# Kernel tuning notes

Hardware: AMD Instinct MI355X
Metric: run time of the kernel (lower is better)

The kernel has to match this reference:

```python
import jax, jax.numpy as jnp
import numpy as np

N = 100000; E = 1600000; F_NODE = 64; F_EDGE = 16
H = 4; C = 32; HC = H * C  # heads=4, per-head out=32, concat dim 128
NG = 64; NCLS = 10
DIMS_IN = [F_NODE, HC, HC]


def _init_params(key):
    ps = {}
    ks = iter(jax.random.split(key, 40))
    for i, din in enumerate(DIMS_IN, 1):
        ps[f"W{i}"] = jax.random.normal(next(ks), (din, HC), jnp.float32) / np.sqrt(din).astype(np.float32)
        ps[f"aS{i}"] = jax.random.normal(next(ks), (H, C), jnp.float32) / np.sqrt(C).astype(np.float32)
        ps[f"aD{i}"] = jax.random.normal(next(ks), (H, C), jnp.float32) / np.sqrt(C).astype(np.float32)
        ps[f"We{i}"] = jax.random.normal(next(ks), (F_EDGE, HC), jnp.float32) / np.sqrt(F_EDGE).astype(np.float32)
        ps[f"aE{i}"] = jax.random.normal(next(ks), (H, C), jnp.float32) / np.sqrt(C).astype(np.float32)
        ps[f"b{i}"] = jnp.zeros((HC,), jnp.float32)
    ps["Wc1"] = jax.random.normal(next(ks), (HC, 128), jnp.float32) / np.sqrt(HC).astype(np.float32)
    ps["bc1"] = jnp.zeros((128,), jnp.float32)
    ps["Wc2"] = jax.random.normal(next(ks), (128, NCLS), jnp.float32) / np.sqrt(128).astype(np.float32)
    ps["bc2"] = jnp.zeros((NCLS,), jnp.float32)
    ps["Wl1"] = jax.random.normal(next(ks), (HC, 64), jnp.float32) / np.sqrt(HC).astype(np.float32)
    ps["bl1"] = jnp.zeros((64,), jnp.float32)
    ps["Wl2"] = jax.random.normal(next(ks), (64, 1), jnp.float32) / np.sqrt(64).astype(np.float32)
    ps["bl2"] = jnp.zeros((1,), jnp.float32)
    return ps


def setup_inputs() -> dict:
    key = jax.random.key(0)
    kx, ke, ki, kb, kp = jax.random.split(key, 5)
    inp = {
        "x": jax.random.normal(kx, (N, F_NODE), jnp.float32),
        "edge_index": jax.random.randint(ki, (2, E), 0, N, dtype=jnp.int64) if jax.config.jax_enable_x64 else jax.random.randint(ki, (2, E), 0, N),
        "edge_attr": jax.random.normal(ke, (E, F_EDGE), jnp.float32),
        "batch": jnp.sort(jax.random.randint(kb, (N,), 0, NG)),
    }
    inp.update(_init_params(kp))
    return inp


def _gat(x, src, dst, ea, W, aS, aD, We, aE, b):
    # One PyG-style GATConv (concat=True, eval mode, self-loops already added).
    n = x.shape[0]
    h = (x @ W).reshape(n, H, C)                    # [N,H,C]
    e = (ea @ We).reshape(-1, H, C)                 # [E',H,C]
    ls = jnp.einsum("nhc,hc->nh", h, aS)            # alpha_src per node
    ld = jnp.einsum("nhc,hc->nh", h, aD)            # alpha_dst per node
    le = jnp.einsum("ehc,hc->eh", e, aE)            # alpha_edge per edge
    logits = jax.nn.leaky_relu(ls[src] + ld[dst] + le, 0.2)  # [E',H]
    m = jax.ops.segment_max(logits, dst, num_segments=n)
    m = jnp.where(jnp.isfinite(m), m, 0.0)          # guard empty segments
    ex = jnp.exp(logits - m[dst])
    den = jax.ops.segment_sum(ex, dst, num_segments=n) + 1e-16
    alpha = ex / den[dst]                           # segment softmax over dst
    out = jax.ops.segment_sum(h[src] * alpha[..., None], dst, num_segments=n)
    return out.reshape(n, HC) + b


def reference(x, edge_index, edge_attr, batch, W1, aS1, aD1, We1, aE1, b1, W2, aS2, aD2, We2, aE2, b2, W3, aS3, aD3, We3, aE3, b3, Wc1, bc1, Wc2, bc2, Wl1, bl1, Wl2, bl2):
    n = x.shape[0]
    loop = jnp.arange(n, dtype=edge_index.dtype)
    src = jnp.concatenate([edge_index[0], loop])
    dst = jnp.concatenate([edge_index[1], loop])
    # self-loop edge_attr filled with mean of edge_attr (PyG fill_value='mean')
    ea = jnp.concatenate([edge_attr, jnp.broadcast_to(edge_attr.mean(0), (n, edge_attr.shape[1]))], 0)
    h = jax.nn.elu(_gat(x, src, dst, ea, W1, aS1, aD1, We1, aE1, b1))
    h = jax.nn.elu(_gat(h, src, dst, ea, W2, aS2, aD2, We2, aE2, b2))
    h = _gat(h, src, dst, ea, W3, aS3, aD3, We3, aE3, b3)
    loc_logits = (jax.nn.relu(h @ Wl1 + bl1) @ Wl2 + bl2)[:, 0]
    cnt = jax.ops.segment_sum(jnp.ones((n,), x.dtype), batch, num_segments=NG)
    gemb = jax.ops.segment_sum(h, batch, num_segments=NG) / jnp.maximum(cnt, 1.0)[:, None]
    class_logits = jax.nn.relu(gemb @ Wc1 + bc1) @ Wc2 + bc2
    return class_logits, loc_logits
```

## Files before the change

kernel.cpp:

```cpp
#include <hip/hip_runtime.h>
#include <math.h>


constexpr int SCAN_TILE = 2048;
constexpr int DEG_CAP = 128;

__global__ void init_cnt_kernel(int* cnt, float* mean_acc, int n) {
  int i = blockIdx.x * blockDim.x + threadIdx.x;
  if (i < n) cnt[i] = 1;
  if (blockIdx.x == 0 && threadIdx.x < 16) mean_acc[threadIdx.x] = 0.f;
}

__global__ void count_kernel(const int* __restrict__ dst, int* cnt, int E) {
  int stride = gridDim.x * blockDim.x;
  for (int e = blockIdx.x * blockDim.x + threadIdx.x; e < E; e += stride)
    atomicAdd(&cnt[dst[e]], 1);
}

__global__ void scan1_kernel(const int* __restrict__ cnt, int* rowptr, int* bsum, int n) {
  __shared__ int part[256];
  int t = threadIdx.x, b = blockIdx.x;
  int base = b * SCAN_TILE + t * 8;
  int v[8];
  int s = 0;
#pragma unroll
  for (int i = 0; i < 8; ++i) {
    int idx = base + i;
    v[i] = (idx < n) ? cnt[idx] : 0;
    s += v[i];
  }
  part[t] = s;
  __syncthreads();
  if (t == 0) {
    int run = 0;
    for (int i = 0; i < 256; ++i) { int x = part[i]; part[i] = run; run += x; }
    bsum[b] = run;
  }
  __syncthreads();
  int run = part[t];
#pragma unroll
  for (int i = 0; i < 8; ++i) {
    int idx = base + i;
    run += v[i];
    if (idx < n) rowptr[idx + 1] = run;
  }
}

__global__ void scan2_kernel(int* bsum, int nb, int* rowptr) {
  if (threadIdx.x == 0 && blockIdx.x == 0) {
    rowptr[0] = 0;
    int run = 0;
    for (int b = 0; b < nb; ++b) { int x = bsum[b]; bsum[b] = run; run += x; }
  }
}

__global__ void scan3_kernel(const int* __restrict__ bsum, int* rowptr, int* cursor, int n) {
  int off = bsum[blockIdx.x];
  int base = blockIdx.x * SCAN_TILE + threadIdx.x * 8;
#pragma unroll
  for (int i = 0; i < 8; ++i) {
    int idx = base + i;
    if (idx < n) {
      int v = rowptr[idx + 1] + off;
      rowptr[idx + 1] = v;
      if (idx + 1 < n) cursor[idx + 1] = v;
    }
  }
  if (blockIdx.x == 0 && threadIdx.x == 0) cursor[0] = 0;
}

__global__ void scatter_kernel(const int* __restrict__ ei, int* cursor,
                               int* esrc, int* eeid, int E, int n) {
  int stride = gridDim.x * blockDim.x;
  int total = E + n;
  for (int i = blockIdx.x * blockDim.x + threadIdx.x; i < total; i += stride) {
    int s, d, id;
    if (i < E) { s = ei[i]; d = ei[E + i]; id = i; }
    else       { s = i - E; d = s; id = E; }
    int pos = atomicAdd(&cursor[d], 1);
    esrc[pos] = s;
    eeid[pos] = id;
  }
}

template <bool MEAN>
__global__ void le_kernel(const float* __restrict__ ea, const float* __restrict__ We,
                          const float* __restrict__ aE, float* __restrict__ le,
                          float* __restrict__ m_acc, int E) {
  __shared__ float wr[16][4];
  int t = threadIdx.x;
  if (t < 64) {
    int f = t >> 2, h = t & 3;
    float s = 0.f;
    for (int c = 0; c < 32; ++c) s += We[f * 128 + h * 32 + c] * aE[h * 32 + c];
    wr[f][h] = s;
  }
  __syncthreads();
  float a[16];
  if (MEAN) {
#pragma unroll
    for (int i = 0; i < 16; ++i) a[i] = 0.f;
  }
  int stride = gridDim.x * blockDim.x;
  for (int e = blockIdx.x * blockDim.x + t; e < E; e += stride) {
    const float4* p = (const float4*)(ea + (size_t)e * 16);
    float4 x0 = p[0], x1 = p[1], x2 = p[2], x3 = p[3];
    float xf[16] = {x0.x, x0.y, x0.z, x0.w, x1.x, x1.y, x1.z, x1.w,
                    x2.x, x2.y, x2.z, x2.w, x3.x, x3.y, x3.z, x3.w};
    if (MEAN) {
#pragma unroll
      for (int i = 0; i < 16; ++i) a[i] += xf[i];
    }
    float oo[4];
#pragma unroll
    for (int h = 0; h < 4; ++h) {
      float s = 0.f;
#pragma unroll
      for (int f = 0; f < 16; ++f) s += xf[f] * wr[f][h];
      oo[h] = s;
    }
    *(float4*)(le + (size_t)e * 4) = make_float4(oo[0], oo[1], oo[2], oo[3]);
  }
  if (MEAN) {
    __shared__ float sm[16];
    if (t < 16) sm[t] = 0.f;
    __syncthreads();
#pragma unroll
    for (int i = 0; i < 16; ++i) atomicAdd(&sm[i], a[i]);
    __syncthreads();
    if (t < 16) atomicAdd(&m_acc[t], sm[t]);
  }
}

__global__ void le_self_kernel(const float* __restrict__ mean_acc, float scale,
                               const float* __restrict__ We, const float* __restrict__ aE,
                               float* __restrict__ le, int E) {
  __shared__ float wr[16][4];
  int t = threadIdx.x;
  if (t < 64) {
    int f = t >> 2, h = t & 3;
    float s = 0.f;
    for (int c = 0; c < 32; ++c) s += We[f * 128 + h * 32 + c] * aE[h * 32 + c];
    wr[f][h] = s;
  }
  __syncthreads();
  if (t < 4) {
    float s = 0.f;
    for (int f = 0; f < 16; ++f) s += mean_acc[f] * scale * wr[f][t];
    le[(size_t)E * 4 + t] = s;
  }
}

template <int K>
__global__ __launch_bounds__(128) void proj_kernel(
    const float* __restrict__ in, const float* __restrict__ W,
    const float* __restrict__ aS, const float* __restrict__ aD,
    float* __restrict__ hp, float* __restrict__ ls, float* __restrict__ ldv, int n) {
  __shared__ float xs[8][K];
  int t = threadIdx.x;
  int base = blockIdx.x * 8;
  for (int idx = t; idx < 8 * K; idx += 128) {
    int r = idx / K, k = idx - r * K;
    int row = base + r;
    xs[r][k] = (row < n) ? in[(size_t)row * K + k] : 0.f;
  }
  __syncthreads();
  float acc[8];
#pragma unroll
  for (int r = 0; r < 8; ++r) acc[r] = 0.f;
  for (int k = 0; k < K; ++k) {
    float w = W[k * 128 + t];
#pragma unroll
    for (int r = 0; r < 8; ++r) acc[r] += xs[r][k] * w;
  }
  float sA = aS[t], sD = aD[t];
  int h = t >> 5;
#pragma unroll
  for (int r = 0; r < 8; ++r) {
    int row = base + r;
    if (row < n) hp[(size_t)row * 128 + t] = acc[r];
    float vS = acc[r] * sA;
    float vD = acc[r] * sD;
#pragma unroll
    for (int off = 1; off < 32; off <<= 1) {
      vS += __shfl_xor(vS, off);
      vD += __shfl_xor(vD, off);
    }
    if ((t & 31) == 0 && row < n) {
      ls[(size_t)row * 4 + h] = vS;
      ldv[(size_t)row * 4 + h] = vD;
    }
  }
}

__global__ __launch_bounds__(256) void agg_kernel(
    const float* __restrict__ hp, const float* __restrict__ ls,
    const float* __restrict__ ldv, const float* __restrict__ le,
    const int* __restrict__ rowptr, const int* __restrict__ esrc,
    const int* __restrict__ eeid, const float* __restrict__ bias,
    float* __restrict__ out, int n, int do_elu) {
  __shared__ float gall[4][DEG_CAP * 4];
  float* gl = gall[threadIdx.x >> 6];
  int wid = (blockIdx.x * blockDim.x + threadIdx.x) >> 6;
  int lane = threadIdx.x & 63;
  if (wid >= n) return;
  int lo = rowptr[wid], hi = rowptr[wid + 1];
  int deg = hi - lo;
  float4 ldn = *(const float4*)(ldv + (size_t)wid * 4);
  int h = lane >> 4;
  int col = lane * 2;
  float ldh = h == 0 ? ldn.x : (h == 1 ? ldn.y : (h == 2 ? ldn.z : ldn.w));
  float a0 = 0.f, a1 = 0.f;

  if (deg <= DEG_CAP) {
    float m0 = -1e30f, m1 = -1e30f, m2 = -1e30f, m3 = -1e30f;
    for (int e = lo + lane, j = lane; e < hi; e += 64, j += 64) {
      int src = esrc[e];
      int id = eeid[e];
      float4 lsv = *(const float4*)(ls + (size_t)src * 4);
      float4 lev = *(const float4*)(le + (size_t)id * 4);
      float g0 = lsv.x + ldn.x + lev.x; g0 = g0 > 0.f ? g0 : 0.2f * g0;
      float g1 = lsv.y + ldn.y + lev.y; g1 = g1 > 0.f ? g1 : 0.2f * g1;
      float g2 = lsv.z + ldn.z + lev.z; g2 = g2 > 0.f ? g2 : 0.2f * g2;
      float g3 = lsv.w + ldn.w + lev.w; g3 = g3 > 0.f ? g3 : 0.2f * g3;
      ((float4*)gl)[j] = make_float4(g0, g1, g2, g3);
      m0 = fmaxf(m0, g0); m1 = fmaxf(m1, g1); m2 = fmaxf(m2, g2); m3 = fmaxf(m3, g3);
    }
#pragma unroll
    for (int off = 1; off < 64; off <<= 1) {
      m0 = fmaxf(m0, __shfl_xor(m0, off));
      m1 = fmaxf(m1, __shfl_xor(m1, off));
      m2 = fmaxf(m2, __shfl_xor(m2, off));
      m3 = fmaxf(m3, __shfl_xor(m3, off));
    }
    if (m0 < -1e29f) m0 = 0.f;
    if (m1 < -1e29f) m1 = 0.f;
    if (m2 < -1e29f) m2 = 0.f;
    if (m3 < -1e29f) m3 = 0.f;
    float mh = h == 0 ? m0 : (h == 1 ? m1 : (h == 2 ? m2 : m3));

    float sacc = 0.f;
    int je = lane & 15;
    for (int j0 = 0; j0 < deg; j0 += 16) {
      int j = j0 + je;
      if (j < deg) {
        float g = gl[j * 4 + h];
        float a = __expf(g - mh);
        gl[j * 4 + h] = a;
        sacc += a;
      }
    }
#pragma unroll
    for (int off = 1; off < 16; off <<= 1) sacc += __shfl_xor(sacc, off);
    float rdh = 1.0f / (sacc + 1e-16f);

    for (int e = lo, j = 0; e < hi; ++e, ++j) {
      int src = esrc[e];
      float alpha = gl[j * 4 + h];
      float2 v = *(const float2*)(hp + (size_t)src * 128 + col);
      a0 += alpha * v.x;
      a1 += alpha * v.y;
    }
    a0 *= rdh;
    a1 *= rdh;
  } else {
    float m0 = -1e30f, m1 = -1e30f, m2 = -1e30f, m3 = -1e30f;
    float s0 = 0.f, s1 = 0.f, s2 = 0.f, s3 = 0.f;
    for (int e = lo + lane; e < hi; e += 64) {
      int src = esrc[e];
      int id = eeid[e];
      float4 lsv = *(const float4*)(ls + (size_t)src * 4);
      float4 lev = *(const float4*)(le + (size_t)id * 4);
      float g0 = lsv.x + ldn.x + lev.x; g0 = g0 > 0.f ? g0 : 0.2f * g0;
      float g1 = lsv.y + ldn.y + lev.y; g1 = g1 > 0.f ? g1 : 0.2f * g1;
      float g2 = lsv.z + ldn.z + lev.z; g2 = g2 > 0.f ? g2 : 0.2f * g2;
      float g3 = lsv.w + ldn.w + lev.w; g3 = g3 > 0.f ? g3 : 0.2f * g3;
      float nm;
      nm = fmaxf(m0, g0); s0 = s0 * __expf(m0 - nm) + __expf(g0 - nm); m0 = nm;
      nm = fmaxf(m1, g1); s1 = s1 * __expf(m1 - nm) + __expf(g1 - nm); m1 = nm;
      nm = fmaxf(m2, g2); s2 = s2 * __expf(m2 - nm) + __expf(g2 - nm); m2 = nm;
      nm = fmaxf(m3, g3); s3 = s3 * __expf(m3 - nm) + __expf(g3 - nm); m3 = nm;
    }
#pragma unroll
    for (int off = 1; off < 64; off <<= 1) {
      float om, os, nm;
      om = __shfl_xor(m0, off); os = __shfl_xor(s0, off);
      nm = fmaxf(m0, om); s0 = s0 * __expf(m0 - nm) + os * __expf(om - nm); m0 = nm;
      om = __shfl_xor(m1, off); os = __shfl_xor(s1, off);
      nm = fmaxf(m1, om); s1 = s1 * __expf(m1 - nm) + os * __expf(om - nm); m1 = nm;
      om = __shfl_xor(m2, off); os = __shfl_xor(s2, off);
      nm = fmaxf(m2, om); s2 = s2 * __expf(m2 - nm) + os * __expf(om - nm); m2 = nm;
      om = __shfl_xor(m3, off); os = __shfl_xor(s3, off);
      nm = fmaxf(m3, om); s3 = s3 * __expf(m3 - nm) + os * __expf(om - nm); m3 = nm;
    }
    if (m0 < -1e29f) m0 = 0.f;
    if (m1 < -1e29f) m1 = 0.f;
    if (m2 < -1e29f) m2 = 0.f;
    if (m3 < -1e29f) m3 = 0.f;
    s0 += 1e-16f; s1 += 1e-16f; s2 += 1e-16f; s3 += 1e-16f;
    float mh = h == 0 ? m0 : (h == 1 ? m1 : (h == 2 ? m2 : m3));
    float rdh = 1.0f / (h == 0 ? s0 : (h == 1 ? s1 : (h == 2 ? s2 : s3)));
    for (int e = lo; e < hi; ++e) {
      int src = esrc[e];
      int id = eeid[e];
      float g = ls[(size_t)src * 4 + h] + ldh + le[(size_t)id * 4 + h];
      g = g > 0.f ? g : 0.2f * g;
      float alpha = __expf(g - mh) * rdh;
      float2 v = *(const float2*)(hp + (size_t)src * 128 + col);
      a0 += alpha * v.x;
      a1 += alpha * v.y;
    }
  }

  float o0 = a0 + bias[col];
  float o1 = a1 + bias[col + 1];
  if (do_elu) {
    o0 = o0 > 0.f ? o0 : expm1f(o0);
    o1 = o1 > 0.f ? o1 : expm1f(o1);
  }
  *(float2*)(out + (size_t)wid * 128 + col) = make_float2(o0, o1);
}

__global__ __launch_bounds__(256) void loc_kernel(
    const float* __restrict__ h, const float* __restrict__ Wl1,
    const float* __restrict__ bl1, const float* __restrict__ Wl2,
    const float* __restrict__ bl2, float* __restrict__ out, int n) {
  int wid = (blockIdx.x * blockDim.x + threadIdx.x) >> 6;
  int lane = threadIdx.x & 63;
  if (wid >= n) return;
  const float* hr = h + (size_t)wid * 128;
  float ac0 = 0.f, ac1 = 0.f, ac2 = 0.f, ac3 = 0.f;
  for (int k = 0; k < 128; k += 4) {
    float4 hv = *(const float4*)(hr + k);
    ac0 += hv.x * Wl1[(k + 0) * 64 + lane];
    ac1 += hv.y * Wl1[(k + 1) * 64 + lane];
    ac2 += hv.z * Wl1[(k + 2) * 64 + lane];
    ac3 += hv.w * Wl1[(k + 3) * 64 + lane];
  }
  float acc = bl1[lane] + ((ac0 + ac1) + (ac2 + ac3));
  acc = fmaxf(acc, 0.f) * Wl2[lane];
#pragma unroll
  for (int off = 1; off < 64; off <<= 1) acc += __shfl_xor(acc, off);
  if (lane == 0) out[wid] = acc + bl2[0];
}

__global__ void zero_gemb_kernel(float* gemb) {
  int i = blockIdx.x * blockDim.x + threadIdx.x;
  if (i < 64 * 128) gemb[i] = 0.f;
}

__global__ __launch_bounds__(128) void pool_kernel(
    const float* __restrict__ h, const int* __restrict__ batch,
    float* __restrict__ gemb, int n) {
  int t = threadIdx.x;
  int base = blockIdx.x * 128;
  int end = base + 128 < n ? base + 128 : n;
  float acc = 0.f;
  int cur = -1;
  for (int node = base; node < end; ++node) {
    int g = batch[node];
    if (g != cur) {
      if (cur >= 0) atomicAdd(&gemb[cur * 128 + t], acc);
      acc = 0.f;
      cur = g;
    }
    acc += h[(size_t)node * 128 + t];
  }
  if (cur >= 0) atomicAdd(&gemb[cur * 128 + t], acc);
}

__global__ __launch_bounds__(128) void class_mlp_kernel(
    const float* __restrict__ gsum, const int* __restrict__ batch,
    const float* __restrict__ Wc1, const float* __restrict__ bc1,
    const float* __restrict__ Wc2, const float* __restrict__ bc2,
    float* __restrict__ out, int n) {
  int g = blockIdx.x;
  int t = threadIdx.x;
  int lo = 0, hi = n;
  while (lo < hi) { int mid = (lo + hi) >> 1; if (batch[mid] < g) lo = mid + 1; else hi = mid; }
  int a = lo, b2 = n;
  while (a < b2) { int mid = (a + b2) >> 1; if (batch[mid] < g + 1) a = mid + 1; else b2 = mid; }
  int cnt = a - lo;
  float denom = cnt > 0 ? (float)cnt : 1.f;
  __shared__ float gemb[128];
  __shared__ float hidl[128];
  gemb[t] = gsum[g * 128 + t] / denom;
  __syncthreads();
  float hid = bc1[t];
  for (int k = 0; k < 128; ++k) hid += gemb[k] * Wc1[k * 128 + t];
  hidl[t] = fmaxf(hid, 0.f);
  __syncthreads();
  if (t < 10) {
    float o = bc2[t];
    for (int k = 0; k < 128; ++k) o += hidl[k] * Wc2[k * 10 + t];
    out[g * 10 + t] = o;
  }
}

extern "C" void kernel_launch(void* const* d_in, const int* in_sizes, int n_in,
                              void* d_out, int out_size, void* d_ws, size_t ws_size,
                              hipStream_t stream) {
  const float* x = (const float*)d_in[0];
  const int* ei = (const int*)d_in[1];
  const float* ea = (const float*)d_in[2];
  const int* batch = (const int*)d_in[3];
  const float* W[3]  = {(const float*)d_in[4],  (const float*)d_in[10], (const float*)d_in[16]};
  const float* aS[3] = {(const float*)d_in[5],  (const float*)d_in[11], (const float*)d_in[17]};
  const float* aD[3] = {(const float*)d_in[6],  (const float*)d_in[12], (const float*)d_in[18]};
  const float* We[3] = {(const float*)d_in[7],  (const float*)d_in[13], (const float*)d_in[19]};
  const float* aE[3] = {(const float*)d_in[8],  (const float*)d_in[14], (const float*)d_in[20]};
  const float* bb[3] = {(const float*)d_in[9],  (const float*)d_in[15], (const float*)d_in[21]};
  const float* Wc1 = (const float*)d_in[22];
  const float* bc1 = (const float*)d_in[23];
  const float* Wc2 = (const float*)d_in[24];
  const float* bc2 = (const float*)d_in[25];
  const float* Wl1 = (const float*)d_in[26];
  const float* bl1 = (const float*)d_in[27];
  const float* Wl2 = (const float*)d_in[28];
  const float* bl2 = (const float*)d_in[29];

  const int N = in_sizes[0] / 64;
  const int E = in_sizes[1] / 2;
  const int EP = E + N;

  char* p = (char*)d_ws;
  auto alloc = [&](size_t bytes) {
    char* r = p;
    p += (bytes + 255) & ~(size_t)255;
    return r;
  };
  float* A      = (float*)alloc((size_t)N * 128 * 4);
  float* hp     = (float*)alloc((size_t)N * 128 * 4);
  float* ls     = (float*)alloc((size_t)N * 4 * 4);
  float* ldv    = (float*)alloc((size_t)N * 4 * 4);
  float* le     = (float*)alloc((size_t)(E + 1) * 4 * 4);
  int* rowptr   = (int*)alloc((size_t)(N + 1) * 4);
  int* cursor   = (int*)alloc((size_t)N * 4);
  int* bsum     = (int*)alloc(256 * 4);
  int* esrc     = (int*)alloc((size_t)EP * 4);
  int* eeid     = (int*)alloc((size_t)EP * 4);
  float* m_acc  = (float*)alloc(16 * 4);
  float* gemb   = (float*)alloc(64 * 128 * 4);

  float* out_cls = (float*)d_out;
  float* out_loc = (float*)d_out + 640;

  int nb = (N + SCAN_TILE - 1) / SCAN_TILE;

  init_cnt_kernel<<<(N + 255) / 256, 256, 0, stream>>>(cursor, m_acc, N);
  count_kernel<<<1024, 256, 0, stream>>>(ei + E, cursor, E);
  scan1_kernel<<<nb, 256, 0, stream>>>(cursor, rowptr, bsum, N);
  scan2_kernel<<<1, 64, 0, stream>>>(bsum, nb, rowptr);
  scan3_kernel<<<nb, 256, 0, stream>>>(bsum, rowptr, cursor, N);
  scatter_kernel<<<2048, 256, 0, stream>>>(ei, cursor, esrc, eeid, E, N);

  for (int l = 0; l < 3; ++l) {
    if (l == 0)
      le_kernel<true><<<2048, 256, 0, stream>>>(ea, We[0], aE[0], le, m_acc, E);
    else
      le_kernel<false><<<2048, 256, 0, stream>>>(ea, We[l], aE[l], le, nullptr, E);
    le_self_kernel<<<1, 64, 0, stream>>>(m_acc, 1.0f / (float)E, We[l], aE[l], le, E);
    if (l == 0)
      proj_kernel<64><<<(N + 7) / 8, 128, 0, stream>>>(x, W[0], aS[0], aD[0], hp, ls, ldv, N);
    else
      proj_kernel<128><<<(N + 7) / 8, 128, 0, stream>>>(A, W[l], aS[l], aD[l], hp, ls, ldv, N);
    agg_kernel<<<(N * 64 + 255) / 256, 256, 0, stream>>>(
        hp, ls, ldv, le, rowptr, esrc, eeid, bb[l], A, N, l < 2 ? 1 : 0);
  }

  loc_kernel<<<(N * 64 + 255) / 256, 256, 0, stream>>>(A, Wl1, bl1, Wl2, bl2, out_loc, N);
  zero_gemb_kernel<<<32, 256, 0, stream>>>(gemb);
  pool_kernel<<<(N + 127) / 128, 128, 0, stream>>>(A, batch, gemb, N);
  class_mlp_kernel<<<64, 128, 0, stream>>>(gemb, batch, Wc1, bc1, Wc2, bc2, out_cls, N);
}
```

Measured before the change: 1.483 ms.

## Fuse per-layer edge logit kernels into one pass and tile loc MLP

Computes the edge-attention logits for all three layers in a single pass over edge_attr, writing three separate le buffers when workspace allows, so edge_attr is read once instead of three times. The self-loop logit kernel now folds We·aE inline instead of going through shared memory. The loc MLP is rewritten as a shared-memory tiled 64-node by 64-hidden GEMM with 4x4 register blocking, replacing one wave per node. The cost is extra workspace for two more le buffers, with the old path kept as a fallback.

```diff
diff --git a/kernel.cpp b/kernel.cpp
--- a/kernel.cpp
+++ b/kernel.cpp
@@ -83,6 +83,81 @@
   }
 }
 
+__global__ void le_all_kernel(
+    const float* __restrict__ ea,
+    const float* __restrict__ We0, const float* __restrict__ aE0,
+    const float* __restrict__ We1, const float* __restrict__ aE1,
+    const float* __restrict__ We2, const float* __restrict__ aE2,
+    float* __restrict__ le0, float* __restrict__ le1, float* __restrict__ le2,
+    float* __restrict__ m_acc, int E) {
+  __shared__ float wr[3][16][4];
+  int t = threadIdx.x;
+  if (t < 192) {
+    int l = t >> 6, r = t & 63, f = r >> 2, hh = r & 3;
+    const float* We = l == 0 ? We0 : (l == 1 ? We1 : We2);
+    const float* aE = l == 0 ? aE0 : (l == 1 ? aE1 : aE2);
+    float s = 0.f;
+    for (int c = 0; c < 32; ++c) s += We[f * 128 + hh * 32 + c] * aE[hh * 32 + c];
+    wr[l][f][hh] = s;
+  }
+  __syncthreads();
+  float a[16];
+#pragma unroll
+  for (int i = 0; i < 16; ++i) a[i] = 0.f;
+  int stride = gridDim.x * blockDim.x;
+  for (int e = blockIdx.x * blockDim.x + t; e < E; e += stride) {
+    const float4* p = (const float4*)(ea + (size_t)e * 16);
+    float4 x0 = p[0], x1 = p[1], x2 = p[2], x3 = p[3];
+    float xf[16] = {x0.x, x0.y, x0.z, x0.w, x1.x, x1.y, x1.z, x1.w,
+                    x2.x, x2.y, x2.z, x2.w, x3.x, x3.y, x3.z, x3.w};
+#pragma unroll
+    for (int i = 0; i < 16; ++i) a[i] += xf[i];
+#pragma unroll
+    for (int l = 0; l < 3; ++l) {
+      float oo[4];
+#pragma unroll
+      for (int hh = 0; hh < 4; ++hh) {
+        float s = 0.f;
+#pragma unroll
+        for (int f = 0; f < 16; ++f) s += xf[f] * wr[l][f][hh];
+        oo[hh] = s;
+      }
+      float* le = l == 0 ? le0 : (l == 1 ? le1 : le2);
+      *(float4*)(le + (size_t)e * 4) = make_float4(oo[0], oo[1], oo[2], oo[3]);
+    }
+  }
+  __shared__ float sm[16];
+  if (t < 16) sm[t] = 0.f;
+  __syncthreads();
+#pragma unroll
+  for (int i = 0; i < 16; ++i) atomicAdd(&sm[i], a[i]);
+  __syncthreads();
+  if (t < 16) atomicAdd(&m_acc[t], sm[t]);
+}
+
+__global__ void le_self_all_kernel(
+    const float* __restrict__ mean_acc, float scale,
+    const float* __restrict__ We0, const float* __restrict__ aE0,
+    const float* __restrict__ We1, const float* __restrict__ aE1,
+    const float* __restrict__ We2, const float* __restrict__ aE2,
+    float* __restrict__ le0, float* __restrict__ le1, float* __restrict__ le2,
+    int E) {
+  int t = threadIdx.x;
+  if (t < 12) {
+    int l = t >> 2, hh = t & 3;
+    const float* We = l == 0 ? We0 : (l == 1 ? We1 : We2);
+    const float* aE = l == 0 ? aE0 : (l == 1 ? aE1 : aE2);
+    float* le = l == 0 ? le0 : (l == 1 ? le1 : le2);
+    float s = 0.f;
+    for (int f = 0; f < 16; ++f) {
+      float w = 0.f;
+      for (int c = 0; c < 32; ++c) w += We[f * 128 + hh * 32 + c] * aE[hh * 32 + c];
+      s += mean_acc[f] * scale * w;
+    }
+    le[(size_t)E * 4 + hh] = s;
+  }
+}
+
 template <bool MEAN>
 __global__ void le_kernel(const float* __restrict__ ea, const float* __restrict__ We,
                           const float* __restrict__ aE, float* __restrict__ le,
@@ -135,18 +210,14 @@
 __global__ void le_self_kernel(const float* __restrict__ mean_acc, float scale,
                                const float* __restrict__ We, const float* __restrict__ aE,
                                float* __restrict__ le, int E) {
-  __shared__ float wr[16][4];
-  int t = threadIdx.x;
-  if (t < 64) {
-    int f = t >> 2, h = t & 3;
-    float s = 0.f;
-    for (int c = 0; c < 32; ++c) s += We[f * 128 + h * 32 + c] * aE[h * 32 + c];
-    wr[f][h] = s;
-  }
-  __syncthreads();
+  int t = threadIdx.x;
   if (t < 4) {
     float s = 0.f;
-    for (int f = 0; f < 16; ++f) s += mean_acc[f] * scale * wr[f][t];
+    for (int f = 0; f < 16; ++f) {
+      float w = 0.f;
+      for (int c = 0; c < 32; ++c) w += We[f * 128 + t * 32 + c] * aE[t * 32 + c];
+      s += mean_acc[f] * scale * w;
+    }
     le[(size_t)E * 4 + t] = s;
   }
 }
@@ -325,23 +396,77 @@
     const float* __restrict__ h, const float* __restrict__ Wl1,
     const float* __restrict__ bl1, const float* __restrict__ Wl2,
     const float* __restrict__ bl2, float* __restrict__ out, int n) {
-  int wid = (blockIdx.x * blockDim.x + threadIdx.x) >> 6;
-  int lane = threadIdx.x & 63;
-  if (wid >= n) return;
-  const float* hr = h + (size_t)wid * 128;
-  float ac0 = 0.f, ac1 = 0.f, ac2 = 0.f, ac3 = 0.f;
-  for (int k = 0; k < 128; k += 4) {
-    float4 hv = *(const float4*)(hr + k);
-    ac0 += hv.x * Wl1[(k + 0) * 64 + lane];
-    ac1 += hv.y * Wl1[(k + 1) * 64 + lane];
-    ac2 += hv.z * Wl1[(k + 2) * 64 + lane];
-    ac3 += hv.w * Wl1[(k + 3) * 64 + lane];
-  }
-  float acc = bl1[lane] + ((ac0 + ac1) + (ac2 + ac3));
-  acc = fmaxf(acc, 0.f) * Wl2[lane];
-#pragma unroll
-  for (int off = 1; off < 64; off <<= 1) acc += __shfl_xor(acc, off);
-  if (lane == 0) out[wid] = acc + bl2[0];
+  __shared__ float hs[32][68];
+  __shared__ float ws[32][68];
+  int t = threadIdx.x;
+  int tx = t & 15;
+  int ty = t >> 4;
+  int nbase = blockIdx.x * 64;
+  float acc[4][4];
+#pragma unroll
+  for (int i = 0; i < 4; ++i)
+#pragma unroll
+    for (int j = 0; j < 4; ++j) acc[i][j] = 0.f;
+
+  for (int kc = 0; kc < 128; kc += 32) {
+    __syncthreads();
+    {
+      int row = t >> 2;
+      int q = t & 3;
+      int node = nbase + row;
+      float4 v0 = make_float4(0.f, 0.f, 0.f, 0.f);
+      float4 v1 = v0;
+      if (node < n) {
+        const float4* src = (const float4*)(h + (size_t)node * 128 + kc);
+        v0 = src[q];
+        v1 = src[q + 4];
+      }
+      int k0 = q * 4;
+      hs[k0 + 0][row] = v0.x; hs[k0 + 1][row] = v0.y;
+      hs[k0 + 2][row] = v0.z; hs[k0 + 3][row] = v0.w;
+      hs[k0 + 16][row] = v1.x; hs[k0 + 17][row] = v1.y;
+      hs[k0 + 18][row] = v1.z; hs[k0 + 19][row] = v1.w;
+    }
+    {
+      const float4* wsrc = (const float4*)(Wl1 + kc * 64);
+#pragma unroll
+      for (int q = 0; q < 2; ++q) {
+        int idx = q * 256 + t;
+        float4 v = wsrc[idx];
+        int k = idx >> 4;
+        int hid = (idx & 15) * 4;
+        *(float4*)&ws[k][hid] = v;
+      }
+    }
+    __syncthreads();
+#pragma unroll
+    for (int k = 0; k < 32; ++k) {
+      float4 hv = *(const float4*)&hs[k][ty * 4];
+      float4 wv = *(const float4*)&ws[k][tx * 4];
+      acc[0][0] += hv.x * wv.x; acc[0][1] += hv.x * wv.y;
+      acc[0][2] += hv.x * wv.z; acc[0][3] += hv.x * wv.w;
+      acc[1][0] += hv.y * wv.x; acc[1][1] += hv.y * wv.y;
+      acc[1][2] += hv.y * wv.z; acc[1][3] += hv.y * wv.w;
+      acc[2][0] += hv.z * wv.x; acc[2][1] += hv.z * wv.y;
+      acc[2][2] += hv.z * wv.z; acc[2][3] += hv.z * wv.w;
+      acc[3][0] += hv.w * wv.x; acc[3][1] += hv.w * wv.y;
+      acc[3][2] += hv.w * wv.z; acc[3][3] += hv.w * wv.w;
+    }
+  }
+  float4 b1 = *(const float4*)(bl1 + tx * 4);
+  float4 w2 = *(const float4*)(Wl2 + tx * 4);
+  float b2v = bl2[0];
+#pragma unroll
+  for (int i = 0; i < 4; ++i) {
+    float s = fmaxf(acc[i][0] + b1.x, 0.f) * w2.x +
+              fmaxf(acc[i][1] + b1.y, 0.f) * w2.y +
+              fmaxf(acc[i][2] + b1.z, 0.f) * w2.z +
+              fmaxf(acc[i][3] + b1.w, 0.f) * w2.w;
+#pragma unroll
+    for (int off = 1; off < 16; off <<= 1) s += __shfl_xor(s, off);
+    int node = nbase + ty * 4 + i;
+    if (tx == 0 && node < n) out[node] = s + b2v;
+  }
 }
 
 __global__ void zero_gemb_kernel(float* gemb) {
@@ -433,7 +558,7 @@
   float* hp     = (float*)alloc((size_t)N * 128 * 4);
   float* ls     = (float*)alloc((size_t)N * 4 * 4);
   float* ldv    = (float*)alloc((size_t)N * 4 * 4);
-  float* le     = (float*)alloc((size_t)(E + 1) * 4 * 4);
+  float* le0    = (float*)alloc((size_t)(E + 1) * 4 * 4);
   int* rowptr   = (int*)alloc((size_t)(N + 1) * 4);
   int* cursor   = (int*)alloc((size_t)N * 4);
   int* bsum     = (int*)alloc(256 * 4);
@@ -441,6 +566,13 @@
   int* eeid     = (int*)alloc((size_t)EP * 4);
   float* m_acc  = (float*)alloc(16 * 4);
   float* gemb   = (float*)alloc(64 * 128 * 4);
+  size_t le_bytes = (((size_t)(E + 1) * 4 * 4) + 255) & ~(size_t)255;
+  float* le1 = nullptr;
+  float* le2 = nullptr;
+  if ((size_t)(p - (char*)d_ws) + 2 * le_bytes <= ws_size) {
+    le1 = (float*)alloc((size_t)(E + 1) * 4 * 4);
+    le2 = (float*)alloc((size_t)(E + 1) * 4 * 4);
+  }
 
   float* out_cls = (float*)d_out;
   float* out_loc = (float*)d_out + 640;
@@ -454,21 +586,32 @@
   scan3_kernel<<<nb, 256, 0, stream>>>(bsum, rowptr, cursor, N);
   scatter_kernel<<<2048, 256, 0, stream>>>(ei, cursor, esrc, eeid, E, N);
 
+  if (le1) {
+    le_all_kernel<<<2048, 256, 0, stream>>>(ea, We[0], aE[0], We[1], aE[1],
+                                            We[2], aE[2], le0, le1, le2, m_acc, E);
+    le_self_all_kernel<<<1, 64, 0, stream>>>(m_acc, 1.0f / (float)E,
+                                             We[0], aE[0], We[1], aE[1],
+                                             We[2], aE[2], le0, le1, le2, E);
+  }
+
   for (int l = 0; l < 3; ++l) {
-    if (l == 0)
-      le_kernel<true><<<2048, 256, 0, stream>>>(ea, We[0], aE[0], le, m_acc, E);
-    else
-      le_kernel<false><<<2048, 256, 0, stream>>>(ea, We[l], aE[l], le, nullptr, E);
-    le_self_kernel<<<1, 64, 0, stream>>>(m_acc, 1.0f / (float)E, We[l], aE[l], le, E);
+    float* leL = l == 0 ? le0 : (l == 1 ? (le1 ? le1 : le0) : (le2 ? le2 : le0));
+    if (!le1) {
+      if (l == 0)
+        le_kernel<true><<<2048, 256, 0, stream>>>(ea, We[0], aE[0], le0, m_acc, E);
+      else
+        le_kernel<false><<<2048, 256, 0, stream>>>(ea, We[l], aE[l], le0, nullptr, E);
+      le_self_kernel<<<1, 64, 0, stream>>>(m_acc, 1.0f / (float)E, We[l], aE[l], le0, E);
+    }
     if (l == 0)
       proj_kernel<64><<<(N + 7) / 8, 128, 0, stream>>>(x, W[0], aS[0], aD[0], hp, ls, ldv, N);
     else
       proj_kernel<128><<<(N + 7) / 8, 128, 0, stream>>>(A, W[l], aS[l], aD[l], hp, ls, ldv, N);
     agg_kernel<<<(N * 64 + 255) / 256, 256, 0, stream>>>(
-        hp, ls, ldv, le, rowptr, esrc, eeid, bb[l], A, N, l < 2 ? 1 : 0);
-  }
-
-  loc_kernel<<<(N * 64 + 255) / 256, 256, 0, stream>>>(A, Wl1, bl1, Wl2, bl2, out_loc, N);
+        hp, ls, ldv, leL, rowptr, esrc, eeid, bb[l], A, N, l < 2 ? 1 : 0);
+  }
+
+  loc_kernel<<<(N + 63) / 64, 256, 0, stream>>>(A, Wl1, bl1, Wl2, bl2, out_loc, N);
   zero_gemb_kernel<<<32, 256, 0, stream>>>(gemb);
   pool_kernel<<<(N + 127) / 128, 128, 0, stream>>>(A, batch, gemb, N);
   class_mlp_kernel<<<64, 128, 0, stream>>>(gemb, batch, Wc1, bc1, Wc2, bc2, out_cls, N);
```

New measurement: 1.456 ms. Within noise of the previous version (-1.8%).
